# Performance work log

Hardware: AMD Instinct MI355X
Metric: run time of the kernel (lower is better)

## Reference

```python
import jax, jax.numpy as jnp
import numpy as np

N = 1024            # samples per branch
C = 64              # num_classes == embedding dim
MARGIN = 15.0       # self.margin and args.margin
LAM = 0.5           # args.lam
PROTOTYPE_POSITION = 1.0  # args.prototype_position
EPS_JS = 1e-8

def _cdist(a, b):
    # torch.cdist(p=2) via the gram trick; clamp for sqrt stability
    d2 = jnp.sum(a * a, axis=1)[:, None] + jnp.sum(b * b, axis=1)[None, :] - 2.0 * (a @ b.T)
    return jnp.sqrt(jnp.maximum(d2, 1e-12))

def _js_matrix(A, B):
    # pairwise Jensen-Shannon divergence: A [NA,C], B [NB,C] -> [NA,NB]
    A = A + EPS_JS
    B = B + EPS_JS
    logM = jnp.log((A[:, None, :] + B[None, :, :]) * 0.5)   # [NA,NB,C]
    kl_am = jnp.sum(A[:, None, :] * (jnp.log(A)[:, None, :] - logM), axis=-1)
    kl_bm = jnp.sum(B[None, :, :] * (jnp.log(B)[None, :, :] - logM), axis=-1)
    return 0.5 * kl_am + 0.5 * kl_bm

def _positive_branch(x, l_soft, x_prob):
    onehot = jnp.eye(C, dtype=x.dtype)
    # JS coefficient is computed via numpy in torch -> constant (no grad)
    js = jax.lax.stop_gradient(1.0 - _js_matrix(x_prob, onehot))       # [N, C]
    diff = x[:, None, :] - onehot * PROTOTYPE_POSITION                 # [N, C, C]
    pos_dist = jnp.sqrt(jnp.maximum(jnp.sum(diff * diff, axis=2), 1e-12))
    return jnp.sum(pos_dist * l_soft * js, axis=1)                     # [N]

def _ood_branch(x, branch_centers):
    d = _cdist(x, branch_centers)                                      # [N, C]
    ood_dist = jnp.maximum(MARGIN - d, 0.0)  # one_hot_labels are all ones
    coffi = jax.lax.stop_gradient(jnp.min(1.0 - ood_dist / MARGIN, axis=1))
    variance = jnp.sum((ood_dist / MARGIN) ** 2, axis=1)
    return variance * coffi                                            # [N]

def setup_inputs():
    key = jax.random.key(0)
    ks = jax.random.split(key, 6)
    x1 = jax.random.normal(ks[0], (N, C), jnp.float32)
    x2 = jax.random.normal(ks[1], (N, C), jnp.float32)
    x_prob1 = jax.nn.softmax(jax.random.normal(ks[2], (N, C), jnp.float32), axis=-1)
    x_prob2 = jax.nn.softmax(jax.random.normal(ks[3], (N, C), jnp.float32), axis=-1)
    l1 = jax.random.uniform(ks[4], (N, C), jnp.float32)
    l1 = l1 / jnp.sum(l1, axis=1, keepdims=True)
    l2 = jax.random.uniform(ks[5], (N, C), jnp.float32)
    l2 = l2 / jnp.sum(l2, axis=1, keepdims=True)
    # args.prototypes: class prototypes at scaled one-hot positions
    branch_centers = jnp.eye(C, dtype=jnp.float32) * PROTOTYPE_POSITION
    return {"x1": x1, "x2": x2, "x_prob1": x_prob1, "x_prob2": x_prob2,
            "l1": l1, "l2": l2, "branch_centers": branch_centers}

def reference(x1, x2, x_prob1, x_prob2, l1, l2, branch_centers):
    # positive loss
    posi = 0.5 * (jnp.sum(_positive_branch(x1, l1, x_prob1))
                  + jnp.sum(_positive_branch(x2, l2, x_prob2)))
    # negative loss
    neg_coffi = 1.0 - l1 @ l2.T                                        # [N, N]
    js = jax.lax.stop_gradient(_js_matrix(x_prob1, x_prob2))           # [N, N]
    ed = _cdist(x1, x2) + 1e-10
    pairs = jnp.maximum(MARGIN - ed, 0.0) * neg_coffi * js
    counts = jnp.sum(pairs > 0, axis=1)
    counts = jnp.where(counts == 0, 1, counts).astype(pairs.dtype)
    nega = jnp.sum(jnp.sum(pairs, axis=1) / counts)
    # ood loss
    ood = 0.5 * (jnp.sum(_ood_branch(x1, branch_centers))
                 + jnp.sum(_ood_branch(x2, branch_centers)))
    loss = posi + nega + LAM * ood
    return (loss, posi, nega)
```

## Files before the change

### kernel.cpp

```cpp
#include <hip/hip_runtime.h>

#define NN 1024
#define CC 64
#define MARGINF 15.0f
#define EPSJ 1e-8f
#define LN2F 0.69314718056f

#define PP_OFF   0
#define OP_OFF   256
#define NS_OFF   512
#define NC_OFF   (512 + 16 * NN)

__global__ __launch_bounds__(256) void neg_kernel(
    const float* __restrict__ x1, const float* __restrict__ x2,
    const float* __restrict__ p1, const float* __restrict__ p2,
    const float* __restrict__ l1, const float* __restrict__ l2,
    float* __restrict__ ws)
{
    __shared__ float sx1[64][36], sp1[64][36], sl1[64][36];
    __shared__ float sx2[64][36], sp2[64][36], sl2[64][36];
    __shared__ float sc1[64], sq1[64], sc2[64], sq2[64];
    __shared__ float spos[4], sood[4];

    const float S_B_CONST = -1.1595029e-5f;
    const float RSB_CONST = 1.00000064f;

    int t  = threadIdx.x;
    int bx = blockIdx.x, by = blockIdx.y;
    int i0 = by * 64, j0 = bx * 64;
    int w    = t >> 6;
    int lane = t & 63;

    {
        const float* xa = (w < 2) ? x1 : x2;
        const float* pa = (w < 2) ? p1 : p2;
        int   base  = (w < 2) ? i0 : j0;
        float* cdst = (w < 2) ? sc1 : sc2;
        float* qdst = (w < 2) ? sq1 : sq2;
        int loc0 = (w & 1) * 32;
        for (int r = 0; r < 32; ++r) {
            int loc = loc0 + r;
            float P  = pa[(base + loc) * CC + lane];
            float xv = xa[(base + loc) * CC + lane];
            float a  = P + EPSJ;
            float al = a * __logf(a);
            float xs = xv * xv;
            #pragma unroll
            for (int m = 32; m >= 1; m >>= 1) {
                al += __shfl_xor(al, m, 64);
                a  += __shfl_xor(a,  m, 64);
                xs += __shfl_xor(xs, m, 64);
            }
            if (lane == 0) { cdst[loc] = al + LN2F * a; qdst[loc] = xs; }
        }
    }

    {
        int b = by * 16 + bx;
        float pacc = 0.0f, oacc = 0.0f;
        #pragma unroll
        for (int k = 0; k < 2; ++k) {
            int job = 8 * b + 2 * w + k;
            int i = job & (NN - 1);
            bool second = job >= NN;
            const float* x = second ? x2 : x1;
            const float* p = second ? p2 : p1;
            const float* l = second ? l2 : l1;
            float P  = p[i * CC + lane];
            float xv = x[i * CC + lane];
            float lv = l[i * CC + lane];
            float A     = P + EPSJ;
            float AlogA = A * __logf(A);
            float tt    = A + EPSJ;
            float tlogt = tt * __logf(tt);
            float xs    = xv * xv;
            float sA = AlogA, rsA = A, V = tlogt, q = xs;
            #pragma unroll
            for (int m = 32; m >= 1; m >>= 1) {
                sA  += __shfl_xor(sA,  m, 64);
                rsA += __shfl_xor(rsA, m, 64);
                V   += __shfl_xor(V,   m, 64);
                q   += __shfl_xor(q,   m, 64);
            }
            float ww = A + (1.0f + EPSJ);
            float sumslogs = V - tlogt + ww * __logf(ww);
            float js_div = 0.5f * (sA + S_B_CONST - sumslogs + LN2F * (rsA + RSB_CONST));
            float js = 1.0f - js_div;
            float pd = sqrtf(fmaxf(q - 2.0f * xv + 1.0f, 1e-12f));
            float posv = pd * lv * js;
            float od  = fmaxf(MARGINF - pd, 0.0f);
            float rr  = od * (1.0f / MARGINF);
            float var = rr * rr;
            float cof = 1.0f - rr;
            #pragma unroll
            for (int m = 32; m >= 1; m >>= 1) {
                posv += __shfl_xor(posv, m, 64);
                var  += __shfl_xor(var,  m, 64);
                cof   = fminf(cof, __shfl_xor(cof, m, 64));
            }
            pacc += posv;
            oacc += var * cof;
        }
        if (lane == 0) { spos[w] = pacc; sood[w] = oacc; }
    }

    int tx = t & 15, ty = t >> 4;
    float K2[4][4];
    float G[4][4];
    float H[4][4];
    #pragma unroll
    for (int r = 0; r < 4; r++)
        #pragma unroll
        for (int s = 0; s < 4; s++) { K2[r][s] = 0.f; G[r][s] = 0.f; H[r][s] = 0.f; }

    for (int ph = 0; ph < 2; ++ph) {
        if (ph) __syncthreads();
        #pragma unroll
        for (int k = 0; k < 2; k++) {
            int f   = t + k * 256;
            int row = f >> 3;
            int col = (f & 7) * 4;
            int ga  = (i0 + row) * CC + ph * 32 + col;
            int gb  = (j0 + row) * CC + ph * 32 + col;
            float4 v;
            v = *(const float4*)&x1[ga];                         *(float4*)&sx1[row][col] = v;
            v = *(const float4*)&p1[ga];
            v.x += EPSJ; v.y += EPSJ; v.z += EPSJ; v.w += EPSJ;  *(float4*)&sp1[row][col] = v;
            v = *(const float4*)&l1[ga];                         *(float4*)&sl1[row][col] = v;
            v = *(const float4*)&x2[gb];                         *(float4*)&sx2[row][col] = v;
            v = *(const float4*)&p2[gb];
            v.x += EPSJ; v.y += EPSJ; v.z += EPSJ; v.w += EPSJ;  *(float4*)&sp2[row][col] = v;
            v = *(const float4*)&l2[gb];                         *(float4*)&sl2[row][col] = v;
        }
        __syncthreads();

        if (ph == 0 && t == 0) {
            ws[PP_OFF + by * 16 + bx] = spos[0] + spos[1] + spos[2] + spos[3];
            ws[OP_OFF + by * 16 + bx] = sood[0] + sood[1] + sood[2] + sood[3];
        }

        for (int cg = 0; cg < 8; ++cg) {
            int c = cg * 4;
            float4 ap[4], ax[4], alv[4], bp[4], bx4[4], blv[4];
            #pragma unroll
            for (int r = 0; r < 4; r++) {
                int ir = ty + 16 * r;
                int jr = tx + 16 * r;
                ap[r]  = *(float4*)&sp1[ir][c];
                ax[r]  = *(float4*)&sx1[ir][c];
                alv[r] = *(float4*)&sl1[ir][c];
                bp[r]  = *(float4*)&sp2[jr][c];
                bx4[r] = *(float4*)&sx2[jr][c];
                blv[r] = *(float4*)&sl2[jr][c];
            }
            #pragma unroll
            for (int r = 0; r < 4; r++) {
                #pragma unroll
                for (int s = 0; s < 4; s++) {
                    float sv;
                    sv = ap[r].x + bp[s].x; K2[r][s] = fmaf(sv, __log2f(sv), K2[r][s]);
                    G[r][s] = fmaf(ax[r].x, bx4[s].x, G[r][s]);
                    H[r][s] = fmaf(alv[r].x, blv[s].x, H[r][s]);
                    sv = ap[r].y + bp[s].y; K2[r][s] = fmaf(sv, __log2f(sv), K2[r][s]);
                    G[r][s] = fmaf(ax[r].y, bx4[s].y, G[r][s]);
                    H[r][s] = fmaf(alv[r].y, blv[s].y, H[r][s]);
                    sv = ap[r].z + bp[s].z; K2[r][s] = fmaf(sv, __log2f(sv), K2[r][s]);
                    G[r][s] = fmaf(ax[r].z, bx4[s].z, G[r][s]);
                    H[r][s] = fmaf(alv[r].z, blv[s].z, H[r][s]);
                    sv = ap[r].w + bp[s].w; K2[r][s] = fmaf(sv, __log2f(sv), K2[r][s]);
                    G[r][s] = fmaf(ax[r].w, bx4[s].w, G[r][s]);
                    H[r][s] = fmaf(alv[r].w, blv[s].w, H[r][s]);
                }
            }
        }
    }

    float* negS = ws + NS_OFF;
    float* negC = ws + NC_OFF;

    #pragma unroll
    for (int r = 0; r < 4; r++) {
        int li = ty + 16 * r;
        int gi = i0 + li;
        float q1v = sq1[li], c1v = sc1[li];
        float psum = 0.0f, pcnt = 0.0f;
        #pragma unroll
        for (int s = 0; s < 4; s++) {
            int lj = tx + 16 * s;
            float ed = sqrtf(fmaxf(q1v + sq2[lj] - 2.0f * G[r][s], 1e-12f)) + 1e-10f;
            float js = 0.5f * (c1v + sc2[lj] - LN2F * K2[r][s]);
            float pair = fmaxf(MARGINF - ed, 0.0f) * (1.0f - H[r][s]) * js;
            psum += pair;
            pcnt += (pair > 0.0f) ? 1.0f : 0.0f;
        }
        #pragma unroll
        for (int m = 1; m <= 8; m <<= 1) {
            psum += __shfl_xor(psum, m, 64);
            pcnt += __shfl_xor(pcnt, m, 64);
        }
        if (tx == 0) {
            negS[gi * 16 + bx] = psum;
            negC[gi * 16 + bx] = pcnt;
        }
    }
}

__global__ __launch_bounds__(1024) void final_kernel(
    const float* __restrict__ ws, float* __restrict__ out)
{
    __shared__ float redv[16], redp[16], redo[16];
    int t = threadIdx.x;
    const float* rs = ws + NS_OFF + t * 16;
    const float* rc = ws + NC_OFF + t * 16;
    float s = 0.0f, c = 0.0f;
    #pragma unroll
    for (int k = 0; k < 4; k++) {
        float4 a = *(const float4*)&rs[k * 4];
        float4 b = *(const float4*)&rc[k * 4];
        s += (a.x + a.y) + (a.z + a.w);
        c += (b.x + b.y) + (b.z + b.w);
    }
    float v = s / fmaxf(c, 1.0f);
    float pp = (t < 256) ? ws[PP_OFF + t] : 0.0f;
    float oo = (t < 256) ? ws[OP_OFF + t] : 0.0f;
    #pragma unroll
    for (int m = 32; m >= 1; m >>= 1) {
        v  += __shfl_xor(v,  m, 64);
        pp += __shfl_xor(pp, m, 64);
        oo += __shfl_xor(oo, m, 64);
    }
    if ((t & 63) == 0) { redv[t >> 6] = v; redp[t >> 6] = pp; redo[t >> 6] = oo; }
    __syncthreads();
    if (t < 16) {
        float rv = redv[t], rp = redp[t], ro = redo[t];
        #pragma unroll
        for (int m = 8; m >= 1; m >>= 1) {
            rv += __shfl_xor(rv, m, 16);
            rp += __shfl_xor(rp, m, 16);
            ro += __shfl_xor(ro, m, 16);
        }
        if (t == 0) {
            float nega = rv;
            float posi = 0.5f * rp;
            float ood  = 0.5f * ro;
            out[0] = posi + nega + 0.5f * ood;
            out[1] = posi;
            out[2] = nega;
        }
    }
}

extern "C" void kernel_launch(void* const* d_in, const int* in_sizes, int n_in,
                              void* d_out, int out_size, void* d_ws, size_t ws_size,
                              hipStream_t stream) {
    const float* x1 = (const float*)d_in[0];
    const float* x2 = (const float*)d_in[1];
    const float* p1 = (const float*)d_in[2];
    const float* p2 = (const float*)d_in[3];
    const float* l1 = (const float*)d_in[4];
    const float* l2 = (const float*)d_in[5];
    float* ws  = (float*)d_ws;
    float* out = (float*)d_out;

    hipLaunchKernelGGL(neg_kernel, dim3(16, 16), dim3(256), 0, stream,
                       x1, x2, p1, p2, l1, l2, ws);
    hipLaunchKernelGGL(final_kernel, dim3(1), dim3(1024), 0, stream, ws, out);
}
```

Before: 105.1 us.

## Double block size to 512 threads and parallelize row-statistics prologue

Blocks grow from 256 to 512 threads, so each thread's register tile in the 64x64 pairwise JS/distance/label-product computation shrinks from 4x4 to 2x4. Each thread also loads less of the shared-memory tile per phase. The row-statistic prologue (entropy and squared-norm sums) now has four threads per row using float4 loads and log2, replacing a serial 32-row loop per wave with 64-lane shuffles. The positive/OOD job loop becomes one job per wave. The aim is more parallelism and latency hiding per block, at the cost of less register reuse of the B-side operands per FMA.

```diff
diff --git a/kernel.cpp b/kernel.cpp
--- a/kernel.cpp
+++ b/kernel.cpp
@@ -11,7 +11,7 @@
 #define NS_OFF   512
 #define NC_OFF   (512 + 16 * NN)
 
-__global__ __launch_bounds__(256) void neg_kernel(
+__global__ __launch_bounds__(512) void neg_kernel(
     const float* __restrict__ x1, const float* __restrict__ x2,
     const float* __restrict__ p1, const float* __restrict__ p2,
     const float* __restrict__ l1, const float* __restrict__ l2,
@@ -20,7 +20,7 @@
     __shared__ float sx1[64][36], sp1[64][36], sl1[64][36];
     __shared__ float sx2[64][36], sp2[64][36], sl2[64][36];
     __shared__ float sc1[64], sq1[64], sc2[64], sq2[64];
-    __shared__ float spos[4], sood[4];
+    __shared__ float spos[8], sood[8];
 
     const float S_B_CONST = -1.1595029e-5f;
     const float RSB_CONST = 1.00000064f;
@@ -32,94 +32,95 @@
     int lane = t & 63;
 
     {
-        const float* xa = (w < 2) ? x1 : x2;
-        const float* pa = (w < 2) ? p1 : p2;
-        int   base  = (w < 2) ? i0 : j0;
-        float* cdst = (w < 2) ? sc1 : sc2;
-        float* qdst = (w < 2) ? sq1 : sq2;
-        int loc0 = (w & 1) * 32;
-        for (int r = 0; r < 32; ++r) {
-            int loc = loc0 + r;
-            float P  = pa[(base + loc) * CC + lane];
-            float xv = xa[(base + loc) * CC + lane];
-            float a  = P + EPSJ;
-            float al = a * __logf(a);
-            float xs = xv * xv;
-            #pragma unroll
-            for (int m = 32; m >= 1; m >>= 1) {
-                al += __shfl_xor(al, m, 64);
-                a  += __shfl_xor(a,  m, 64);
-                xs += __shfl_xor(xs, m, 64);
-            }
-            if (lane == 0) { cdst[loc] = al + LN2F * a; qdst[loc] = xs; }
+        int row = t >> 2;
+        int q4  = t & 3;
+        bool side1 = row < 64;
+        const float* pa = side1 ? p1 : p2;
+        const float* xa = side1 ? x1 : x2;
+        int grow = side1 ? (i0 + row) : (j0 + (row - 64));
+        const float* prow = pa + grow * CC + q4 * 16;
+        const float* xrow = xa + grow * CC + q4 * 16;
+        float al2 = 0.0f, asum = 0.0f, xs = 0.0f;
+        #pragma unroll
+        for (int k = 0; k < 4; k++) {
+            float4 pv = *(const float4*)&prow[k * 4];
+            float4 xv = *(const float4*)&xrow[k * 4];
+            float a;
+            a = pv.x + EPSJ; al2 = fmaf(a, __log2f(a), al2); asum += a;
+            a = pv.y + EPSJ; al2 = fmaf(a, __log2f(a), al2); asum += a;
+            a = pv.z + EPSJ; al2 = fmaf(a, __log2f(a), al2); asum += a;
+            a = pv.w + EPSJ; al2 = fmaf(a, __log2f(a), al2); asum += a;
+            xs = fmaf(xv.x, xv.x, xs); xs = fmaf(xv.y, xv.y, xs);
+            xs = fmaf(xv.z, xv.z, xs); xs = fmaf(xv.w, xv.w, xs);
+        }
+        #pragma unroll
+        for (int m = 1; m <= 2; m <<= 1) {
+            al2  += __shfl_xor(al2,  m, 64);
+            asum += __shfl_xor(asum, m, 64);
+            xs   += __shfl_xor(xs,   m, 64);
+        }
+        if (q4 == 0) {
+            float* cd = side1 ? sc1 : sc2;
+            float* qd = side1 ? sq1 : sq2;
+            cd[row & 63] = LN2F * (al2 + asum);
+            qd[row & 63] = xs;
         }
     }
 
     {
-        int b = by * 16 + bx;
-        float pacc = 0.0f, oacc = 0.0f;
-        #pragma unroll
-        for (int k = 0; k < 2; ++k) {
-            int job = 8 * b + 2 * w + k;
-            int i = job & (NN - 1);
-            bool second = job >= NN;
-            const float* x = second ? x2 : x1;
-            const float* p = second ? p2 : p1;
-            const float* l = second ? l2 : l1;
-            float P  = p[i * CC + lane];
-            float xv = x[i * CC + lane];
-            float lv = l[i * CC + lane];
-            float A     = P + EPSJ;
-            float AlogA = A * __logf(A);
-            float tt    = A + EPSJ;
-            float tlogt = tt * __logf(tt);
-            float xs    = xv * xv;
-            float sA = AlogA, rsA = A, V = tlogt, q = xs;
-            #pragma unroll
-            for (int m = 32; m >= 1; m >>= 1) {
-                sA  += __shfl_xor(sA,  m, 64);
-                rsA += __shfl_xor(rsA, m, 64);
-                V   += __shfl_xor(V,   m, 64);
-                q   += __shfl_xor(q,   m, 64);
-            }
-            float ww = A + (1.0f + EPSJ);
-            float sumslogs = V - tlogt + ww * __logf(ww);
-            float js_div = 0.5f * (sA + S_B_CONST - sumslogs + LN2F * (rsA + RSB_CONST));
-            float js = 1.0f - js_div;
-            float pd = sqrtf(fmaxf(q - 2.0f * xv + 1.0f, 1e-12f));
-            float posv = pd * lv * js;
-            float od  = fmaxf(MARGINF - pd, 0.0f);
-            float rr  = od * (1.0f / MARGINF);
-            float var = rr * rr;
-            float cof = 1.0f - rr;
-            #pragma unroll
-            for (int m = 32; m >= 1; m >>= 1) {
-                posv += __shfl_xor(posv, m, 64);
-                var  += __shfl_xor(var,  m, 64);
-                cof   = fminf(cof, __shfl_xor(cof, m, 64));
-            }
-            pacc += posv;
-            oacc += var * cof;
-        }
-        if (lane == 0) { spos[w] = pacc; sood[w] = oacc; }
+        int job = 8 * (by * 16 + bx) + w;
+        int i = job & (NN - 1);
+        bool second = job >= NN;
+        const float* x = second ? x2 : x1;
+        const float* p = second ? p2 : p1;
+        const float* l = second ? l2 : l1;
+        float P  = p[i * CC + lane];
+        float xv = x[i * CC + lane];
+        float lv = l[i * CC + lane];
+        float A     = P + EPSJ;
+        float AlogA = A * __logf(A);
+        float tt    = A + EPSJ;
+        float tlogt = tt * __logf(tt);
+        float xs    = xv * xv;
+        float sA = AlogA, rsA = A, V = tlogt, q = xs;
+        #pragma unroll
+        for (int m = 32; m >= 1; m >>= 1) {
+            sA  += __shfl_xor(sA,  m, 64);
+            rsA += __shfl_xor(rsA, m, 64);
+            V   += __shfl_xor(V,   m, 64);
+            q   += __shfl_xor(q,   m, 64);
+        }
+        float ww = A + (1.0f + EPSJ);
+        float sumslogs = V - tlogt + ww * __logf(ww);
+        float js_div = 0.5f * (sA + S_B_CONST - sumslogs + LN2F * (rsA + RSB_CONST));
+        float js = 1.0f - js_div;
+        float pd = sqrtf(fmaxf(q - 2.0f * xv + 1.0f, 1e-12f));
+        float posv = pd * lv * js;
+        float od  = fmaxf(MARGINF - pd, 0.0f);
+        float rr  = od * (1.0f / MARGINF);
+        float var = rr * rr;
+        float cof = 1.0f - rr;
+        #pragma unroll
+        for (int m = 32; m >= 1; m >>= 1) {
+            posv += __shfl_xor(posv, m, 64);
+            var  += __shfl_xor(var,  m, 64);
+            cof   = fminf(cof, __shfl_xor(cof, m, 64));
+        }
+        if (lane == 0) { spos[w] = posv; sood[w] = var * cof; }
     }
 
     int tx = t & 15, ty = t >> 4;
-    float K2[4][4];
-    float G[4][4];
-    float H[4][4];
-    #pragma unroll
-    for (int r = 0; r < 4; r++)
+    float K2[2][4], G[2][4], H[2][4];
+    #pragma unroll
+    for (int r = 0; r < 2; r++)
         #pragma unroll
         for (int s = 0; s < 4; s++) { K2[r][s] = 0.f; G[r][s] = 0.f; H[r][s] = 0.f; }
 
     for (int ph = 0; ph < 2; ++ph) {
         if (ph) __syncthreads();
-        #pragma unroll
-        for (int k = 0; k < 2; k++) {
-            int f   = t + k * 256;
-            int row = f >> 3;
-            int col = (f & 7) * 4;
+        {
+            int row = t >> 3;
+            int col = (t & 7) * 4;
             int ga  = (i0 + row) * CC + ph * 32 + col;
             int gb  = (j0 + row) * CC + ph * 32 + col;
             float4 v;
@@ -135,26 +136,31 @@
         __syncthreads();
 
         if (ph == 0 && t == 0) {
-            ws[PP_OFF + by * 16 + bx] = spos[0] + spos[1] + spos[2] + spos[3];
-            ws[OP_OFF + by * 16 + bx] = sood[0] + sood[1] + sood[2] + sood[3];
+            ws[PP_OFF + by * 16 + bx] = spos[0] + spos[1] + spos[2] + spos[3]
+                                      + spos[4] + spos[5] + spos[6] + spos[7];
+            ws[OP_OFF + by * 16 + bx] = sood[0] + sood[1] + sood[2] + sood[3]
+                                      + sood[4] + sood[5] + sood[6] + sood[7];
         }
 
         for (int cg = 0; cg < 8; ++cg) {
             int c = cg * 4;
-            float4 ap[4], ax[4], alv[4], bp[4], bx4[4], blv[4];
+            float4 ap[2], ax[2], alv[2], bp[4], bx4[4], blv[4];
             #pragma unroll
-            for (int r = 0; r < 4; r++) {
-                int ir = ty + 16 * r;
-                int jr = tx + 16 * r;
+            for (int r = 0; r < 2; r++) {
+                int ir = ty + 32 * r;
                 ap[r]  = *(float4*)&sp1[ir][c];
                 ax[r]  = *(float4*)&sx1[ir][c];
                 alv[r] = *(float4*)&sl1[ir][c];
-                bp[r]  = *(float4*)&sp2[jr][c];
-                bx4[r] = *(float4*)&sx2[jr][c];
-                blv[r] = *(float4*)&sl2[jr][c];
             }
             #pragma unroll
-            for (int r = 0; r < 4; r++) {
+            for (int s = 0; s < 4; s++) {
+                int jr = tx + 16 * s;
+                bp[s]  = *(float4*)&sp2[jr][c];
+                bx4[s] = *(float4*)&sx2[jr][c];
+                blv[s] = *(float4*)&sl2[jr][c];
+            }
+            #pragma unroll
+            for (int r = 0; r < 2; r++) {
                 #pragma unroll
                 for (int s = 0; s < 4; s++) {
                     float sv;
@@ -179,8 +185,8 @@
     float* negC = ws + NC_OFF;
 
     #pragma unroll
-    for (int r = 0; r < 4; r++) {
-        int li = ty + 16 * r;
+    for (int r = 0; r < 2; r++) {
+        int li = ty + 32 * r;
         int gi = i0 + li;
         float q1v = sq1[li], c1v = sc1[li];
         float psum = 0.0f, pcnt = 0.0f;
@@ -262,7 +268,7 @@
     float* ws  = (float*)d_ws;
     float* out = (float*)d_out;
 
-    hipLaunchKernelGGL(neg_kernel, dim3(16, 16), dim3(256), 0, stream,
+    hipLaunchKernelGGL(neg_kernel, dim3(16, 16), dim3(512), 0, stream,
                        x1, x2, p1, p2, l1, l2, ws);
     hipLaunchKernelGGL(final_kernel, dim3(1), dim3(1024), 0, stream, ws, out);
 }
```

Result: faster. 85.24 us (-18.9%).
